# Optimization experiments

Measured on AMD Instinct MI355X. Metric: run time of the kernel, lower is better.

Reference implementation:

```python
import jax, jax.numpy as jnp
import numpy as np

BIT = 8      # shared-exponent mantissa bits (bf_conf.*_bit)
GSZ = 36     # block size (bf_conf.*_sz)


def bfp_quantize(x, bit=BIT, sz=GSZ):
    """Block floating point: groups of `sz` consecutive elements share one
    exponent e = floor(log2(max|x|)); each element keeps `bit` mantissa bits."""
    shape = x.shape
    flat = x.reshape(-1)
    n = flat.shape[0]
    pad = (-n) % sz
    flat = jnp.pad(flat, (0, pad))
    g = flat.reshape(-1, sz)                                   # [G, sz]
    maxabs = jnp.max(jnp.abs(g), axis=1, keepdims=True)
    e = jnp.floor(jnp.log2(jnp.where(maxabs > 0, maxabs, 1.0)))
    scale = jnp.exp2(e - (bit - 1))                            # lsb of shared-exp format
    q = jnp.round(g / scale) * scale
    q = jnp.where(maxabs > 0, q, 0.0)
    return q.reshape(-1)[:n].reshape(shape)


def setup_inputs() -> dict:
    key = jax.random.key(0)
    k1, k2, k3 = jax.random.split(key, 3)
    B, Cin, Cout, H, W, K = 16, 32, 32, 224, 224, 3
    x = jax.random.normal(k1, (B, Cin, H, W), dtype=jnp.float32)
    fan_in = Cin * K * K
    bound = 1.0 / np.sqrt(fan_in)
    weight = jax.random.uniform(k2, (Cout, Cin, K, K), jnp.float32, -bound, bound)
    bias = jax.random.uniform(k3, (Cout,), jnp.float32, -bound, bound)
    return {"x": x, "weight": weight, "bias": bias}


def reference(x, weight, bias):
    xq = bfp_quantize(x)          # f_i
    wq = bfp_quantize(weight)     # f_w
    out = jax.lax.conv_general_dilated(
        xq, wq,
        window_strides=(1, 1),
        padding=((1, 1), (1, 1)),
        rhs_dilation=(1, 1),
        feature_group_count=1,
        dimension_numbers=("NCHW", "OIHW", "NCHW"),
    )
    out = out + bias[None, :, None, None]
    out = bfp_quantize(out)       # f_o
    return out
```

## Files before the change

kernel.cpp:

```cpp
#include <hip/hip_runtime.h>
#include <hip/hip_bf16.h>

#define GSZ 36
static const int NX  = 16 * 32 * 224 * 224;
static const int NX4 = NX / 4;
static const int NW  = 32 * 32 * 3 * 3;
static const int GXN = (NX + GSZ - 1) / GSZ;
static const int HWp = 224 * 224;

typedef short bf16x8 __attribute__((ext_vector_type(8)));
typedef float f32x4  __attribute__((ext_vector_type(4)));

__device__ __forceinline__ unsigned div36(unsigned n) {
    return (unsigned)(((unsigned long long)n * 954437177ull) >> 35);
}
__device__ __forceinline__ float scale_from_max(float m) {
    int e = (int)((__float_as_uint(m) >> 23) & 0xffu) - 127;
    return __uint_as_float((unsigned)(e + 120) << 23);
}
__device__ __forceinline__ float inv_from_scale(float s) {
    return __uint_as_float(0x7F000000u - __float_as_uint(s));
}
__device__ __forceinline__ unsigned short f2bf(float f) {
    return (unsigned short)(__float_as_uint(f) >> 16);
}

__global__ void k_quant_wt(const float* __restrict__ w, unsigned short* __restrict__ wt) {
    int g = threadIdx.x;
    int base = g * GSZ;
    float v[GSZ];
    const float4* p = reinterpret_cast<const float4*>(w + base);
    #pragma unroll
    for (int i = 0; i < 9; ++i) {
        float4 t = p[i];
        v[4*i+0] = t.x; v[4*i+1] = t.y; v[4*i+2] = t.z; v[4*i+3] = t.w;
    }
    float m = 0.0f;
    #pragma unroll
    for (int i = 0; i < GSZ; ++i) m = fmaxf(m, fabsf(v[i]));
    if (m > 0.0f) {
        float s = scale_from_max(m), inv = inv_from_scale(s);
        #pragma unroll
        for (int i = 0; i < GSZ; ++i) v[i] = rintf(v[i] * inv) * s;
    }
    #pragma unroll
    for (int i = 0; i < GSZ; ++i) {
        int f = base + i;
        int co = f / 288, rem = f - co * 288;
        int ci = rem / 9, s = rem - ci * 9;
        wt[s * 1024 + co * 32 + ci] = f2bf(v[i]);
    }
}

#define TSTR 452
__global__ __launch_bounds__(256, 4) void k_quant_x_fused(const float* __restrict__ x,
                                                          unsigned short* __restrict__ xt) {
    __shared__ __align__(16) unsigned char raw[32 * TSTR * 2];
    unsigned short* tile = reinterpret_cast<unsigned short*>(raw);
    float* pmax = reinterpret_cast<float*>(raw);
    __shared__ float scl[32 * 14];

    int t = threadIdx.x;
    int b = blockIdx.y, hp = blockIdx.x;
    int F0 = (b * 32) * HWp + hp * 448;

    int c4  = t & 127;
    int ciB = t >> 7;

    f32x4 v[16];
    #pragma unroll
    for (int j = 0; j < 16; ++j) {
        int ci = ciB + 2 * j;
        int F = F0 + ci * HWp;
        int r = F - 36 * (int)div36((unsigned)F);
        int f4 = (int)(((unsigned)(F - r)) >> 2) + c4;
        f32x4 tv = {0.f, 0.f, 0.f, 0.f};
        if ((unsigned)f4 < (unsigned)NX4)
            tv = reinterpret_cast<const f32x4*>(x)[f4];
        v[j] = tv;
        pmax[ci * 128 + c4] = fmaxf(fmaxf(fabsf(tv[0]), fabsf(tv[1])),
                                    fmaxf(fabsf(tv[2]), fabsf(tv[3])));
    }
    __syncthreads();

    #pragma unroll
    for (int it = 0; it < 2; ++it) {
        int task = t + 256 * it;
        if (task < 448) {
            int ci = (task * 2341) >> 15;
            int gi = task - ci * 14;
            const float* pp = &pmax[ci * 128 + 9 * gi];
            float m = pp[0];
            #pragma unroll
            for (int i = 1; i < 9; ++i) m = fmaxf(m, pp[i]);
            scl[task] = (m > 0.f) ? scale_from_max(m) : 0.f;
        }
    }
    __syncthreads();

    int gi4 = (c4 * 57) >> 9;
    #pragma unroll
    for (int j = 0; j < 16; ++j) {
        int ci = ciB + 2 * j;
        int F = F0 + ci * HWp;
        int r = F - 36 * (int)div36((unsigned)F);
        int rel = 4 * c4 - r;
        if ((unsigned)rel < 448u) {
            float s = scl[ci * 14 + gi4];
            f32x4 q = v[j];
            if (s > 0.f) {
                float inv = inv_from_scale(s);
                #pragma unroll
                for (int k = 0; k < 4; ++k) q[k] = rintf(q[k] * inv) * s;
            } else {
                q = f32x4{0.f, 0.f, 0.f, 0.f};
            }
            uint2 o;
            o.x = (unsigned)f2bf(q[0]) | ((unsigned)f2bf(q[1]) << 16);
            o.y = (unsigned)f2bf(q[2]) | ((unsigned)f2bf(q[3]) << 16);
            *reinterpret_cast<uint2*>(&tile[ci * TSTR + rel]) = o;
        }
    }
    __syncthreads();

    unsigned short* ob = xt + ((size_t)b * HWp + hp * 448) * 32;
    for (int j = 0; j < 7; ++j) {
        int qd = t + 256 * j;
        int px = qd >> 2;
        int c0 = (qd & 3) * 8;
        unsigned uu[4];
        #pragma unroll
        for (int p = 0; p < 4; ++p) {
            unsigned short lo = tile[(c0 + 2 * p) * TSTR + px];
            unsigned short hi = tile[(c0 + 2 * p + 1) * TSTR + px];
            uu[p] = (unsigned)lo | ((unsigned)hi << 16);
        }
        *reinterpret_cast<uint4*>(ob + (size_t)px * 32 + c0) =
            make_uint4(uu[0], uu[1], uu[2], uu[3]);
    }
}

#define PXS 40
__global__ __launch_bounds__(256, 2) void k_conv_mfma(const unsigned short* __restrict__ xt,
                                                      const unsigned short* __restrict__ wt,
                                                      const float* __restrict__ bias,
                                                      float* __restrict__ out) {
    __shared__ __align__(16) unsigned short xs[18 * 34 * PXS];

    int tid  = threadIdx.x;
    int lane = tid & 63;
    int wid  = tid >> 6;
    int b  = blockIdx.z;
    int h0 = blockIdx.y * 16;
    int w0 = blockIdx.x * 32;

    const unsigned short* xb = xt + (size_t)b * HWp * 32;
    #pragma unroll
    for (int k = 0; k < 10; ++k) {
        int q = tid + k * 256;
        if (q < 2448) {
            int r = q / 136;
            int rem = q - r * 136;
            int p = rem >> 2, ch = rem & 3;
            int gh = h0 + r - 1, gw = w0 + p - 1;
            uint4 val = make_uint4(0u, 0u, 0u, 0u);
            if ((unsigned)gh < 224u && (unsigned)gw < 224u)
                val = *reinterpret_cast<const uint4*>(xb + ((size_t)(gh * 224 + gw)) * 32 + ch * 8);
            *reinterpret_cast<uint4*>(&xs[(r * 34 + p) * PXS + ch * 8]) = val;
        }
    }

    bf16x8 Wf[9][2];
    #pragma unroll
    for (int s = 0; s < 9; ++s)
        #pragma unroll
        for (int hf = 0; hf < 2; ++hf)
            Wf[s][hf] = *reinterpret_cast<const bf16x8*>(
                wt + s * 1024 + (hf * 16 + (lane & 15)) * 32 + (lane >> 4) * 8);

    int m4 = (lane >> 4) << 2;
    f32x4 acc[8][2];
    {
        f32x4 b0, b1;
        #pragma unroll
        for (int r = 0; r < 4; ++r) {
            b0[r] = bias[m4 + r];
            b1[r] = bias[16 + m4 + r];
        }
        #pragma unroll
        for (int g = 0; g < 8; ++g) { acc[g][0] = b0; acc[g][1] = b1; }
    }

    __syncthreads();

    int row4 = wid << 2;
    int kchunk = (lane >> 4) << 3;
    #pragma unroll
    for (int s = 0; s < 9; ++s) {
        int kh = s / 3, kw = s - kh * 3;
        #pragma unroll
        for (int g = 0; g < 8; ++g) {
            int row = row4 + (g >> 1);
            int col = ((g & 1) << 4) + (lane & 15);
            bf16x8 X = *reinterpret_cast<const bf16x8*>(
                &xs[((row + kh) * 34 + col + kw) * PXS + kchunk]);
            acc[g][0] = __builtin_amdgcn_mfma_f32_16x16x32_bf16(Wf[s][0], X, acc[g][0], 0, 0, 0);
            acc[g][1] = __builtin_amdgcn_mfma_f32_16x16x32_bf16(Wf[s][1], X, acc[g][1], 0, 0, 0);
        }
    }

    int pxl = lane & 15;
    #pragma unroll
    for (int g = 0; g < 8; ++g) {
        int h = h0 + row4 + (g >> 1);
        int wl = w0 + ((g & 1) << 4) + pxl;
        size_t base = (size_t)(b * 32) * HWp + h * 224 + wl;
        #pragma unroll
        for (int hf = 0; hf < 2; ++hf)
            #pragma unroll
            for (int r = 0; r < 4; ++r)
                out[base + (size_t)((hf << 4) + m4 + r) * HWp] = acc[g][hf][r];
    }
}

__global__ __launch_bounds__(256, 4) void k_quant_out(float* __restrict__ buf) {
    __shared__ float lds[4 * 2304];
    int t = threadIdx.x, lane = t & 63, wid = t >> 6;
    int gbase = (blockIdx.x * 4 + wid) * 64;
    int f4base = gbase * 9;

    #pragma unroll
    for (int i = 0; i < 9; ++i) {
        int f4 = f4base + i * 64 + lane;
        float4 v = make_float4(0.f, 0.f, 0.f, 0.f);
        if ((unsigned)f4 < (unsigned)NX4) v = reinterpret_cast<const float4*>(buf)[f4];
        *reinterpret_cast<float4*>(&lds[wid * 2304 + (i * 64 + lane) * 4]) = v;
    }
    __syncthreads();

    if (gbase + lane < GXN) {
        float* p = &lds[wid * 2304 + lane * 36];
        f32x4 vv[9];
        #pragma unroll
        for (int i = 0; i < 9; ++i) vv[i] = *reinterpret_cast<f32x4*>(p + 4 * i);
        float m = 0.f;
        #pragma unroll
        for (int i = 0; i < 9; ++i)
            #pragma unroll
            for (int k = 0; k < 4; ++k) m = fmaxf(m, fabsf(vv[i][k]));
        if (m > 0.f) {
            float s = scale_from_max(m), inv = inv_from_scale(s);
            #pragma unroll
            for (int i = 0; i < 9; ++i) {
                #pragma unroll
                for (int k = 0; k < 4; ++k) vv[i][k] = rintf(vv[i][k] * inv) * s;
                *reinterpret_cast<f32x4*>(p + 4 * i) = vv[i];
            }
        }
    }
    __syncthreads();

    #pragma unroll
    for (int i = 0; i < 9; ++i) {
        int f4 = f4base + i * 64 + lane;
        if ((unsigned)f4 < (unsigned)NX4)
            reinterpret_cast<float4*>(buf)[f4] =
                *reinterpret_cast<float4*>(&lds[wid * 2304 + (i * 64 + lane) * 4]);
    }
}

extern "C" void kernel_launch(void* const* d_in, const int* in_sizes, int n_in,
                              void* d_out, int out_size, void* d_ws, size_t ws_size,
                              hipStream_t stream) {
    (void)in_sizes; (void)n_in; (void)out_size; (void)ws_size;
    const float* x    = (const float*)d_in[0];
    const float* w    = (const float*)d_in[1];
    const float* bias = (const float*)d_in[2];
    float* out        = (float*)d_out;

    unsigned short* xt = (unsigned short*)d_ws;
    unsigned short* wt = xt + NX;

    k_quant_wt<<<1, 256, 0, stream>>>(w, wt);
    k_quant_x_fused<<<dim3(112, 16), 256, 0, stream>>>(x, xt);
    k_conv_mfma<<<dim3(7, 14, 16), 256, 0, stream>>>(xt, wt, bias, out);
    k_quant_out<<<2788, 256, 0, stream>>>(out);
}
```

Before: 247.4 us.

## Replace LDS staging in output quantizer with wave-shuffle group max reduction

The output block-quantization kernel no longer stages each wave's 64 groups through shared memory. Each 63-lane slice of a wave now loads seven 36-element groups directly as float4 vectors. The group max is reduced across the 9 lanes of each group with cyclic shuffles, and the quantized values are written back in place. This removes LDS traffic and both barriers, at the cost of leaving one lane in 64 idle and adding shuffle instructions. The grid shrinks because each wave now handles 112 groups.

After: 246.9 us. About the same (-0.2%).

```diff
diff --git a/kernel.cpp b/kernel.cpp
--- a/kernel.cpp
+++ b/kernel.cpp
@@ -223,49 +223,39 @@
     }
 }
 
-__global__ __launch_bounds__(256, 4) void k_quant_out(float* __restrict__ buf) {
-    __shared__ float lds[4 * 2304];
+#define QOG 112
+__global__ __launch_bounds__(256) void k_quant_out(float* __restrict__ buf) {
     int t = threadIdx.x, lane = t & 63, wid = t >> 6;
-    int gbase = (blockIdx.x * 4 + wid) * 64;
-    int f4base = gbase * 9;
-
-    #pragma unroll
-    for (int i = 0; i < 9; ++i) {
-        int f4 = f4base + i * 64 + lane;
-        float4 v = make_float4(0.f, 0.f, 0.f, 0.f);
-        if ((unsigned)f4 < (unsigned)NX4) v = reinterpret_cast<const float4*>(buf)[f4];
-        *reinterpret_cast<float4*>(&lds[wid * 2304 + (i * 64 + lane) * 4]) = v;
-    }
-    __syncthreads();
-
-    if (gbase + lane < GXN) {
-        float* p = &lds[wid * 2304 + lane * 36];
-        f32x4 vv[9];
-        #pragma unroll
-        for (int i = 0; i < 9; ++i) vv[i] = *reinterpret_cast<f32x4*>(p + 4 * i);
-        float m = 0.f;
-        #pragma unroll
-        for (int i = 0; i < 9; ++i)
-            #pragma unroll
-            for (int k = 0; k < 4; ++k) m = fmaxf(m, fabsf(vv[i][k]));
+    int s9 = (lane * 57) >> 9;
+    int p9 = lane - s9 * 9;
+    bool active = lane < 63;
+
+    int src[4];
+    #pragma unroll
+    for (int k = 0; k < 4; ++k) {
+        int rot = 1 << k;
+        int pp = p9 + rot; if (pp >= 9) pp -= 9;
+        src[k] = active ? (s9 * 9 + pp) : 63;
+    }
+
+    int wave_g = (blockIdx.x * 4 + wid) * QOG;
+    #pragma unroll 4
+    for (int i = 0; i < 16; ++i) {
+        int f4 = (wave_g + 7 * i) * 9 + lane;
+        bool ld = active && (unsigned)f4 < (unsigned)NX4;
+        f32x4 v = {0.f, 0.f, 0.f, 0.f};
+        if (ld) v = reinterpret_cast<const f32x4*>(buf)[f4];
+        float m = fmaxf(fmaxf(fabsf(v[0]), fabsf(v[1])),
+                        fmaxf(fabsf(v[2]), fabsf(v[3])));
+        #pragma unroll
+        for (int k = 0; k < 4; ++k)
+            m = fmaxf(m, __shfl(m, src[k]));
         if (m > 0.f) {
             float s = scale_from_max(m), inv = inv_from_scale(s);
             #pragma unroll
-            for (int i = 0; i < 9; ++i) {
-                #pragma unroll
-                for (int k = 0; k < 4; ++k) vv[i][k] = rintf(vv[i][k] * inv) * s;
-                *reinterpret_cast<f32x4*>(p + 4 * i) = vv[i];
-            }
-        }
-    }
-    __syncthreads();
-
-    #pragma unroll
-    for (int i = 0; i < 9; ++i) {
-        int f4 = f4base + i * 64 + lane;
-        if ((unsigned)f4 < (unsigned)NX4)
-            reinterpret_cast<float4*>(buf)[f4] =
-                *reinterpret_cast<float4*>(&lds[wid * 2304 + (i * 64 + lane) * 4]);
+            for (int k = 0; k < 4; ++k) v[k] = rintf(v[k] * inv) * s;
+        }
+        if (ld) reinterpret_cast<f32x4*>(buf)[f4] = v;
     }
 }
 
@@ -284,5 +274,5 @@
     k_quant_wt<<<1, 256, 0, stream>>>(w, wt);
     k_quant_x_fused<<<dim3(112, 16), 256, 0, stream>>>(x, xt);
     k_conv_mfma<<<dim3(7, 14, 16), 256, 0, stream>>>(xt, wt, bias, out);
-    k_quant_out<<<2788, 256, 0, stream>>>(out);
-}
+    k_quant_out<<<1593, 256, 0, stream>>>(out);
+}
```

## Fuse output BFP quantization into conv epilogue with boundary-group fixup kernel

Applied to the files above, without the earlier changes.

Each conv block now computes two full output rows for all 32 channels, stages the results in LDS, and quantizes every 36-element group that lies entirely inside its slab before writing to global memory. Groups that straddle slab boundaries are left unquantized and handled by a small fixup kernel that re-reads and quantizes only those groups. This removes the separate full read-modify-write pass over the output tensor. In exchange it adds a larger LDS footprint and halo overhead (4 input rows per 2 output rows), a different tiling with 7 fragments per wave, and extra launch ordering for the fixup.

Result: no change. 249.1 us (+0.7%).

```diff
diff --git a/kernel.cpp b/kernel.cpp
--- a/kernel.cpp
+++ b/kernel.cpp
@@ -141,32 +141,44 @@
 }
 
 #define PXS 40
-__global__ __launch_bounds__(256, 2) void k_conv_mfma(const unsigned short* __restrict__ xt,
-                                                      const unsigned short* __restrict__ wt,
-                                                      const float* __restrict__ bias,
-                                                      float* __restrict__ out) {
-    __shared__ __align__(16) unsigned short xs[18 * 34 * PXS];
+#define COS 452
+__global__ __launch_bounds__(256, 2) void k_conv_q(const unsigned short* __restrict__ xt,
+                                                   const unsigned short* __restrict__ wt,
+                                                   const float* __restrict__ bias,
+                                                   float* __restrict__ out) {
+    __shared__ __align__(16) unsigned char lraw[4 * 226 * PXS * 2];
+    unsigned short* xs = reinterpret_cast<unsigned short*>(lraw);
+    float* ot = reinterpret_cast<float*>(lraw);
+    __shared__ float scl[32 * 12];
+    __shared__ int rel0s[32], bnds[32];
 
     int tid  = threadIdx.x;
     int lane = tid & 63;
     int wid  = tid >> 6;
-    int b  = blockIdx.z;
-    int h0 = blockIdx.y * 16;
-    int w0 = blockIdx.x * 32;
+    int hpair = blockIdx.x;
+    int b     = blockIdx.y;
+    int h0 = hpair * 2;
+
+    if (tid < 32) {
+        int T = (b * 32 + tid) * HWp + hpair * 448;
+        int r36 = T - 36 * (int)div36((unsigned)T);
+        int rel0 = r36 ? 36 - r36 : 0;
+        rel0s[tid] = rel0;
+        bnds[tid] = rel0 + 36 * (int)div36((unsigned)(448 - rel0));
+    }
 
     const unsigned short* xb = xt + (size_t)b * HWp * 32;
-    #pragma unroll
-    for (int k = 0; k < 10; ++k) {
+    for (int k = 0; k < 15; ++k) {
         int q = tid + k * 256;
-        if (q < 2448) {
-            int r = q / 136;
-            int rem = q - r * 136;
+        if (q < 3616) {
+            int r = ((q >> 3) * 145) >> 14;
+            int rem = q - r * 904;
             int p = rem >> 2, ch = rem & 3;
-            int gh = h0 + r - 1, gw = w0 + p - 1;
+            int gh = h0 - 1 + r, gw = p - 1;
             uint4 val = make_uint4(0u, 0u, 0u, 0u);
             if ((unsigned)gh < 224u && (unsigned)gw < 224u)
                 val = *reinterpret_cast<const uint4*>(xb + ((size_t)(gh * 224 + gw)) * 32 + ch * 8);
-            *reinterpret_cast<uint4*>(&xs[(r * 34 + p) * PXS + ch * 8]) = val;
+            *reinterpret_cast<uint4*>(&xs[(r * 226 + p) * PXS + ch * 8]) = val;
         }
     }
 
@@ -179,7 +191,7 @@
                 wt + s * 1024 + (hf * 16 + (lane & 15)) * 32 + (lane >> 4) * 8);
 
     int m4 = (lane >> 4) << 2;
-    f32x4 acc[8][2];
+    f32x4 acc[7][2];
     {
         f32x4 b0, b1;
         #pragma unroll
@@ -188,84 +200,117 @@
             b1[r] = bias[16 + m4 + r];
         }
         #pragma unroll
-        for (int g = 0; g < 8; ++g) { acc[g][0] = b0; acc[g][1] = b1; }
-    }
-
-    __syncthreads();
-
-    int row4 = wid << 2;
+        for (int i = 0; i < 7; ++i) { acc[i][0] = b0; acc[i][1] = b1; }
+    }
+
+    __syncthreads();
+
+    int l15 = lane & 15;
     int kchunk = (lane >> 4) << 3;
     #pragma unroll
     for (int s = 0; s < 9; ++s) {
         int kh = s / 3, kw = s - kh * 3;
         #pragma unroll
-        for (int g = 0; g < 8; ++g) {
-            int row = row4 + (g >> 1);
-            int col = ((g & 1) << 4) + (lane & 15);
+        for (int i = 0; i < 7; ++i) {
+            int f = wid * 7 + i;
+            int row = (f >= 14) ? 1 : 0;
+            int colf = (f - 14 * row) << 4;
             bf16x8 X = *reinterpret_cast<const bf16x8*>(
-                &xs[((row + kh) * 34 + col + kw) * PXS + kchunk]);
-            acc[g][0] = __builtin_amdgcn_mfma_f32_16x16x32_bf16(Wf[s][0], X, acc[g][0], 0, 0, 0);
-            acc[g][1] = __builtin_amdgcn_mfma_f32_16x16x32_bf16(Wf[s][1], X, acc[g][1], 0, 0, 0);
-        }
-    }
-
-    int pxl = lane & 15;
-    #pragma unroll
-    for (int g = 0; g < 8; ++g) {
-        int h = h0 + row4 + (g >> 1);
-        int wl = w0 + ((g & 1) << 4) + pxl;
-        size_t base = (size_t)(b * 32) * HWp + h * 224 + wl;
+                &xs[((row + kh) * 226 + colf + l15 + kw) * PXS + kchunk]);
+            acc[i][0] = __builtin_amdgcn_mfma_f32_16x16x32_bf16(Wf[s][0], X, acc[i][0], 0, 0, 0);
+            acc[i][1] = __builtin_amdgcn_mfma_f32_16x16x32_bf16(Wf[s][1], X, acc[i][1], 0, 0, 0);
+        }
+    }
+    __syncthreads();
+
+    #pragma unroll
+    for (int i = 0; i < 7; ++i) {
+        int f = wid * 7 + i;
+        int row = (f >= 14) ? 1 : 0;
+        int px = row * 224 + ((f - 14 * row) << 4) + l15;
         #pragma unroll
         for (int hf = 0; hf < 2; ++hf)
             #pragma unroll
             for (int r = 0; r < 4; ++r)
-                out[base + (size_t)((hf << 4) + m4 + r) * HWp] = acc[g][hf][r];
-    }
-}
-
-__global__ __launch_bounds__(256, 4) void k_quant_out(float* __restrict__ buf) {
-    __shared__ float lds[4 * 2304];
-    int t = threadIdx.x, lane = t & 63, wid = t >> 6;
-    int gbase = (blockIdx.x * 4 + wid) * 64;
-    int f4base = gbase * 9;
-
-    #pragma unroll
-    for (int i = 0; i < 9; ++i) {
-        int f4 = f4base + i * 64 + lane;
-        float4 v = make_float4(0.f, 0.f, 0.f, 0.f);
-        if ((unsigned)f4 < (unsigned)NX4) v = reinterpret_cast<const float4*>(buf)[f4];
-        *reinterpret_cast<float4*>(&lds[wid * 2304 + (i * 64 + lane) * 4]) = v;
-    }
-    __syncthreads();
-
-    if (gbase + lane < GXN) {
-        float* p = &lds[wid * 2304 + lane * 36];
-        f32x4 vv[9];
-        #pragma unroll
-        for (int i = 0; i < 9; ++i) vv[i] = *reinterpret_cast<f32x4*>(p + 4 * i);
-        float m = 0.f;
-        #pragma unroll
-        for (int i = 0; i < 9; ++i)
+                ot[(hf * 16 + m4 + r) * COS + px] = acc[i][hf][r];
+    }
+    __syncthreads();
+
+    #pragma unroll
+    for (int it = 0; it < 2; ++it) {
+        int task = tid + it * 256;
+        if (task < 384) {
+            int co = ((task >> 2) * 683) >> 11;
+            int k = task - co * 12;
+            int base = rel0s[co] + 36 * k;
+            if (base < bnds[co]) {
+                const float* pp = &ot[co * COS + base];
+                float m = 0.f;
+                #pragma unroll
+                for (int i = 0; i < 9; ++i) {
+                    f32x4 vv = *reinterpret_cast<const f32x4*>(pp + 4 * i);
+                    m = fmaxf(m, fmaxf(fmaxf(fabsf(vv[0]), fabsf(vv[1])),
+                                       fmaxf(fabsf(vv[2]), fabsf(vv[3]))));
+                }
+                scl[co * 12 + k] = (m > 0.f) ? scale_from_max(m) : 0.f;
+            }
+        }
+    }
+    __syncthreads();
+
+    float* ob = out + (size_t)(b * 32) * HWp + h0 * 224;
+    #pragma unroll
+    for (int j = 0; j < 14; ++j) {
+        int idx = tid + j * 256;
+        int co = ((idx >> 4) * 2341) >> 14;
+        int c4 = idx - co * 112;
+        int px0 = c4 * 4;
+        f32x4 v = *reinterpret_cast<const f32x4*>(&ot[co * COS + px0]);
+        int rz = px0 - rel0s[co];
+        if ((unsigned)rz < (unsigned)(bnds[co] - rel0s[co])) {
+            int k = (int)div36((unsigned)rz);
+            float s = scl[co * 12 + k];
+            if (s > 0.f) {
+                float inv = inv_from_scale(s);
+                #pragma unroll
+                for (int e = 0; e < 4; ++e) v[e] = rintf(v[e] * inv) * s;
+            } else {
+                v = f32x4{0.f, 0.f, 0.f, 0.f};
+            }
+        }
+        *reinterpret_cast<f32x4*>(ob + (size_t)co * HWp + px0) = v;
+    }
+}
+
+__global__ __launch_bounds__(256) void k_fixup(float* __restrict__ buf) {
+    int i = blockIdx.x * 256 + threadIdx.x;
+    if (i >= 50976) return;
+    const unsigned long long SP =
+        12ull | (24ull << 7) | (37ull << 14) | (49ull << 21) |
+        (62ull << 28) | (74ull << 35) | (87ull << 42) | (99ull << 49);
+    int g = (i >> 3) * 112 + (int)((SP >> (7 * (i & 7))) & 127ull);
+    if (g >= GXN) return;
+    int f4 = 9 * g;
+    f32x4 v[9];
+    float m = 0.f;
+    #pragma unroll
+    for (int k = 0; k < 9; ++k) {
+        f32x4 tv = {0.f, 0.f, 0.f, 0.f};
+        if ((unsigned)(f4 + k) < (unsigned)NX4)
+            tv = reinterpret_cast<const f32x4*>(buf)[f4 + k];
+        v[k] = tv;
+        m = fmaxf(m, fmaxf(fmaxf(fabsf(tv[0]), fabsf(tv[1])),
+                           fmaxf(fabsf(tv[2]), fabsf(tv[3]))));
+    }
+    if (m > 0.f) {
+        float s = scale_from_max(m), inv = inv_from_scale(s);
+        #pragma unroll
+        for (int k = 0; k < 9; ++k) {
             #pragma unroll
-            for (int k = 0; k < 4; ++k) m = fmaxf(m, fabsf(vv[i][k]));
-        if (m > 0.f) {
-            float s = scale_from_max(m), inv = inv_from_scale(s);
-            #pragma unroll
-            for (int i = 0; i < 9; ++i) {
-                #pragma unroll
-                for (int k = 0; k < 4; ++k) vv[i][k] = rintf(vv[i][k] * inv) * s;
-                *reinterpret_cast<f32x4*>(p + 4 * i) = vv[i];
-            }
-        }
-    }
-    __syncthreads();
-
-    #pragma unroll
-    for (int i = 0; i < 9; ++i) {
-        int f4 = f4base + i * 64 + lane;
-        if ((unsigned)f4 < (unsigned)NX4)
-            reinterpret_cast<float4*>(buf)[f4] =
-                *reinterpret_cast<float4*>(&lds[wid * 2304 + (i * 64 + lane) * 4]);
+            for (int e = 0; e < 4; ++e) v[k][e] = rintf(v[k][e] * inv) * s;
+            if ((unsigned)(f4 + k) < (unsigned)NX4)
+                reinterpret_cast<f32x4*>(buf)[f4 + k] = v[k];
+        }
     }
 }
 
@@ -283,6 +328,6 @@
 
     k_quant_wt<<<1, 256, 0, stream>>>(w, wt);
     k_quant_x_fused<<<dim3(112, 16), 256, 0, stream>>>(x, xt);
-    k_conv_mfma<<<dim3(7, 14, 16), 256, 0, stream>>>(xt, wt, bias, out);
-    k_quant_out<<<2788, 256, 0, stream>>>(out);
-}
+    k_conv_q<<<dim3(112, 16), 256, 0, stream>>>(xt, wt, bias, out);
+    k_fixup<<<200, 256, 0, stream>>>(out);
+}
```
